# Kernel tuning notes

Hardware: AMD Instinct MI355X
Metric: run time of the kernel (lower is better)

Reference implementation:

```python
import jax, jax.numpy as jnp
import numpy as np

N_NODES = 100000


def _sage_conv(x, edge_index, W_l, W_r, b):
    # PyG SAGEConv (mean aggr): out_i = lin_l(mean_{j in N(i)} x_j) + lin_r(x_i)
    src, dst = edge_index[0], edge_index[1]
    msg = x[src]  # [E, d] gather
    agg_sum = jax.ops.segment_sum(msg, dst, num_segments=N_NODES)  # [N, d]
    deg = jax.ops.segment_sum(jnp.ones((src.shape[0],), x.dtype), dst, num_segments=N_NODES)
    agg = agg_sum / jnp.maximum(deg, 1.0)[:, None]  # mean aggregation
    return agg @ W_l.T + b + x @ W_r.T


def setup_inputs() -> dict:
    key = jax.random.key(0)
    k = jax.random.split(key, 8)
    d_in, hidden, out = 64, 128, 128
    x = jax.random.normal(k[0], (N_NODES, d_in), dtype=jnp.float32)
    edge_index = jax.random.randint(k[1], (2, 1600000), 0, N_NODES, dtype=jnp.int64)
    s1 = 1.0 / np.sqrt(d_in)
    s2 = 1.0 / np.sqrt(hidden)
    return {
        "x": x,
        "edge_index": edge_index,
        "W1_l": jax.random.uniform(k[2], (hidden, d_in), jnp.float32, -s1, s1),
        "W1_r": jax.random.uniform(k[3], (hidden, d_in), jnp.float32, -s1, s1),
        "b1": jnp.zeros((hidden,), jnp.float32),
        "W2_l": jax.random.uniform(k[4], (out, hidden), jnp.float32, -s2, s2),
        "W2_r": jax.random.uniform(k[5], (out, hidden), jnp.float32, -s2, s2),
        "b2": jnp.zeros((out,), jnp.float32),
    }


def reference(x, edge_index, W1_l, W1_r, b1, W2_l, W2_r, b2):
    h = jax.nn.relu(_sage_conv(x, edge_index, W1_l, W1_r, b1))
    return _sage_conv(h, edge_index, W2_l, W2_r, b2)
```

## Files before the change

kernel.cpp:

```cpp
#include <hip/hip_runtime.h>

#define NN 100000
#define NE 1600000
#define SCAN_BLK 2048

#define BSH 9
#define NBUCK2 ((NN + 511) / 512)
#define CHUNK 8192
#define NCHK ((NE + CHUNK - 1) / CHUNK)
#define L2T (NBUCK2 * NCHK)
#define NSTRIP (NN / 32)

using bf16x8 = __attribute__((ext_vector_type(8))) short;
using f32x16 = __attribute__((ext_vector_type(16))) float;

__device__ __forceinline__ unsigned short f2bf(float f) {
    unsigned u = __float_as_uint(f);
    u += 0x7FFFu + ((u >> 16) & 1u);
    return (unsigned short)(u >> 16);
}
__device__ __forceinline__ float bf2f(unsigned short h) {
    return __uint_as_float(((unsigned)h) << 16);
}

__global__ __launch_bounds__(256) void hist2_kernel(const int* __restrict__ dst,
                                                    int* __restrict__ histm) {
    __shared__ int lh[256];
    int blk = blockIdx.x, tid = threadIdx.x;
    lh[tid] = 0;
    __syncthreads();
    int base = blk * CHUNK;
#pragma unroll
    for (int t = 0; t < CHUNK / 256; t++) {
        int e = base + t * 256 + tid;
        if (e < NE) atomicAdd(&lh[dst[e] >> BSH], 1);
    }
    __syncthreads();
    if (tid < NBUCK2) histm[tid * NCHK + blk] = lh[tid];
}

__global__ __launch_bounds__(256) void scan1_kernel(int* __restrict__ data,
                                                    int* __restrict__ bsums, int L) {
    __shared__ int s[256];
    int bid = blockIdx.x, tid = threadIdx.x;
    int base = bid * SCAN_BLK + tid * 8;
    int v[8];
    int sum = 0;
#pragma unroll
    for (int t = 0; t < 8; t++) {
        int idx = base + t;
        v[t] = (idx < L) ? data[idx] : 0;
        sum += v[t];
    }
    s[tid] = sum;
    __syncthreads();
    for (int off = 1; off < 256; off <<= 1) {
        int val = (tid >= off) ? s[tid - off] : 0;
        __syncthreads();
        s[tid] += val;
        __syncthreads();
    }
    int excl = s[tid] - sum;
    if (tid == 255) bsums[bid] = s[255];
    int run = excl;
#pragma unroll
    for (int t = 0; t < 8; t++) {
        int idx = base + t;
        if (idx < L) data[idx] = run;
        run += v[t];
    }
}

__global__ __launch_bounds__(64) void scan2_kernel(int* __restrict__ bsums, int n) {
    int tid = threadIdx.x;
    int orig = (tid < n) ? bsums[tid] : 0;
    int v = orig;
    for (int off = 1; off < 64; off <<= 1) {
        int nb = __shfl_up(v, off, 64);
        if (tid >= off) v += nb;
    }
    if (tid < n) bsums[tid] = v - orig;
}

__global__ __launch_bounds__(256) void scan_add_kernel(int* __restrict__ data,
                                                       const int* __restrict__ bsums, int L) {
    int i = blockIdx.x * 256 + threadIdx.x;
    if (i < L) data[i] += bsums[i / SCAN_BLK];
}

__global__ __launch_bounds__(256) void scatter2_kernel(const int* __restrict__ src,
                                                       const int* __restrict__ dst,
                                                       const int* __restrict__ histm,
                                                       int* __restrict__ tmp) {
    __shared__ int lcur[256];
    int blk = blockIdx.x, tid = threadIdx.x;
    if (tid < NBUCK2) lcur[tid] = histm[tid * NCHK + blk];
    __syncthreads();
    int base = blk * CHUNK;
#pragma unroll
    for (int t = 0; t < CHUNK / 256; t++) {
        int e = base + t * 256 + tid;
        if (e < NE) {
            int d = dst[e];
            int p = atomicAdd(&lcur[d >> BSH], 1);
            tmp[p] = src[e] | ((d & 511) << 17);
        }
    }
}

__global__ __launch_bounds__(256) void count_place_kernel(const int* __restrict__ histm,
                                                          const int* __restrict__ tmp,
                                                          int* __restrict__ rowptr,
                                                          int* __restrict__ esrc) {
    __shared__ int cnt[512];
    __shared__ int s[256];
    int b = blockIdx.x, tid = threadIdx.x;
    int beg = histm[b * NCHK];
    int end = (b == NBUCK2 - 1) ? NE : histm[(b + 1) * NCHK];

    cnt[tid] = 0; cnt[tid + 256] = 0;
    __syncthreads();
    for (int e = beg + tid; e < end; e += 256)
        atomicAdd(&cnt[tmp[e] >> 17], 1);
    __syncthreads();

    int c0 = cnt[2 * tid], c1 = cnt[2 * tid + 1];
    int sum = c0 + c1;
    s[tid] = sum;
    __syncthreads();
    for (int off = 1; off < 256; off <<= 1) {
        int val = (tid >= off) ? s[tid - off] : 0;
        __syncthreads();
        s[tid] += val;
        __syncthreads();
    }
    int o0 = beg + s[tid] - sum;
    int o1 = o0 + c0;
    cnt[2 * tid] = o0;
    cnt[2 * tid + 1] = o1;
    int node0 = (b << BSH) + 2 * tid;
    if (node0 < NN)     rowptr[node0]     = o0;
    if (node0 + 1 < NN) rowptr[node0 + 1] = o1;
    if (b == 0 && tid == 0) rowptr[NN] = NE;
    __syncthreads();

    for (int e = beg + tid; e < end; e += 256) {
        int v = tmp[e];
        int p = atomicAdd(&cnt[v >> 17], 1);
        esrc[p] = v & 0x1FFFF;
    }
}

__global__ __launch_bounds__(256) void cvt_kernel(const float* __restrict__ in,
                                                  unsigned short* __restrict__ out, int n4) {
    int i = blockIdx.x * 256 + threadIdx.x;
    if (i < n4) {
        float4 f = ((const float4*)in)[i];
        ((ushort4*)out)[i] = make_ushort4(f2bf(f.x), f2bf(f.y), f2bf(f.z), f2bf(f.w));
    }
}

__global__ __launch_bounds__(256) void agg64_kernel(const unsigned short* __restrict__ feat,
                                                    const int* __restrict__ rowptr,
                                                    const int* __restrict__ esrc,
                                                    unsigned short* __restrict__ agg) {
    int node = blockIdx.x * 4 + (threadIdx.x >> 6);
    int lane = threadIdx.x & 63;
    int es = lane >> 3;
    int fi = lane & 7;
    int beg = rowptr[node], end = rowptr[node + 1];

    float ax[8];
#pragma unroll
    for (int i = 0; i < 8; i++) ax[i] = 0.0f;

    int e = beg;
    for (; e + 15 < end; e += 16) {
        int sA = esrc[e + es];
        int sB = esrc[e + 8 + es];
        bf16x8 uA = *(const bf16x8*)(feat + (size_t)sA * 64 + fi * 8);
        bf16x8 uB = *(const bf16x8*)(feat + (size_t)sB * 64 + fi * 8);
#pragma unroll
        for (int i = 0; i < 8; i++)
            ax[i] += bf2f((unsigned short)uA[i]) + bf2f((unsigned short)uB[i]);
    }
    if (e + 7 < end) {
        int s = esrc[e + es];
        bf16x8 u = *(const bf16x8*)(feat + (size_t)s * 64 + fi * 8);
#pragma unroll
        for (int i = 0; i < 8; i++) ax[i] += bf2f((unsigned short)u[i]);
        e += 8;
    }
    if (es < end - e) {
        int s = esrc[e + es];
        bf16x8 u = *(const bf16x8*)(feat + (size_t)s * 64 + fi * 8);
#pragma unroll
        for (int i = 0; i < 8; i++) ax[i] += bf2f((unsigned short)u[i]);
    }

#pragma unroll
    for (int i = 0; i < 8; i++) {
        ax[i] += __shfl_xor(ax[i], 8);
        ax[i] += __shfl_xor(ax[i], 16);
        ax[i] += __shfl_xor(ax[i], 32);
    }
    if (es == 0) {
        float inv = 1.0f / fmaxf((float)(end - beg), 1.0f);
        bf16x8 o;
#pragma unroll
        for (int i = 0; i < 8; i++) o[i] = (short)f2bf(ax[i] * inv);
        *(bf16x8*)(agg + (size_t)node * 64 + fi * 8) = o;
    }
}

__global__ __launch_bounds__(256) void agg128_kernel(const unsigned short* __restrict__ feat,
                                                     const int* __restrict__ rowptr,
                                                     const int* __restrict__ esrc,
                                                     unsigned short* __restrict__ agg) {
    int node = blockIdx.x * 4 + (threadIdx.x >> 6);
    int lane = threadIdx.x & 63;
    int es = lane >> 4;
    int fi = lane & 15;
    int beg = rowptr[node], end = rowptr[node + 1];

    float ax[8];
#pragma unroll
    for (int i = 0; i < 8; i++) ax[i] = 0.0f;

    int e = beg;
    for (; e + 15 < end; e += 16) {
        int s0 = esrc[e + es];
        int s1 = esrc[e + 4 + es];
        int s2 = esrc[e + 8 + es];
        int s3 = esrc[e + 12 + es];
        bf16x8 u0 = *(const bf16x8*)(feat + (size_t)s0 * 128 + fi * 8);
        bf16x8 u1 = *(const bf16x8*)(feat + (size_t)s1 * 128 + fi * 8);
        bf16x8 u2 = *(const bf16x8*)(feat + (size_t)s2 * 128 + fi * 8);
        bf16x8 u3 = *(const bf16x8*)(feat + (size_t)s3 * 128 + fi * 8);
#pragma unroll
        for (int i = 0; i < 8; i++)
            ax[i] += (bf2f((unsigned short)u0[i]) + bf2f((unsigned short)u1[i])) +
                     (bf2f((unsigned short)u2[i]) + bf2f((unsigned short)u3[i]));
    }
    for (; e + 3 < end; e += 4) {
        int s = esrc[e + es];
        bf16x8 u = *(const bf16x8*)(feat + (size_t)s * 128 + fi * 8);
#pragma unroll
        for (int i = 0; i < 8; i++) ax[i] += bf2f((unsigned short)u[i]);
    }
    if (es < end - e) {
        int s = esrc[e + es];
        bf16x8 u = *(const bf16x8*)(feat + (size_t)s * 128 + fi * 8);
#pragma unroll
        for (int i = 0; i < 8; i++) ax[i] += bf2f((unsigned short)u[i]);
    }

#pragma unroll
    for (int i = 0; i < 8; i++) {
        ax[i] += __shfl_xor(ax[i], 16);
        ax[i] += __shfl_xor(ax[i], 32);
    }
    if (es == 0) {
        float inv = 1.0f / fmaxf((float)(end - beg), 1.0f);
        bf16x8 o;
#pragma unroll
        for (int i = 0; i < 8; i++) o[i] = (short)f2bf(ax[i] * inv);
        *(bf16x8*)(agg + (size_t)node * 128 + fi * 8) = o;
    }
}

template <int K, bool RELU, bool OUTBF>
__global__ __launch_bounds__(256) void gemm_mfma_kernel(
    const unsigned short* __restrict__ A1,
    const unsigned short* __restrict__ A2,
    const unsigned short* __restrict__ Wa,
    const unsigned short* __restrict__ Wb,
    const float* __restrict__ bias,
    void* __restrict__ outv) {
    int strip = blockIdx.x * 4 + (threadIdx.x >> 6);
    if (strip >= NSTRIP) return;
    const int lane = threadIdx.x & 63;
    const int m = lane & 31;
    const int half = lane >> 5;
    const int base = strip * 32;

    f32x16 acc[4];
#pragma unroll
    for (int nb = 0; nb < 4; ++nb)
#pragma unroll
        for (int r = 0; r < 16; ++r) acc[nb][r] = 0.0f;

    const unsigned short* ar1 = A1 + (size_t)(base + m) * K + half * 8;
    const unsigned short* ar2 = A2 + (size_t)(base + m) * K + half * 8;
#pragma unroll
    for (int kc = 0; kc < K; kc += 16) {
        bf16x8 a = *(const bf16x8*)(ar1 + kc);
#pragma unroll
        for (int nb = 0; nb < 4; ++nb) {
            bf16x8 b = *(const bf16x8*)(Wa + (size_t)(nb * 32 + m) * K + kc + half * 8);
            acc[nb] = __builtin_amdgcn_mfma_f32_32x32x16_bf16(a, b, acc[nb], 0, 0, 0);
        }
    }
#pragma unroll
    for (int kc = 0; kc < K; kc += 16) {
        bf16x8 a = *(const bf16x8*)(ar2 + kc);
#pragma unroll
        for (int nb = 0; nb < 4; ++nb) {
            bf16x8 b = *(const bf16x8*)(Wb + (size_t)(nb * 32 + m) * K + kc + half * 8);
            acc[nb] = __builtin_amdgcn_mfma_f32_32x32x16_bf16(a, b, acc[nb], 0, 0, 0);
        }
    }

#pragma unroll
    for (int nb = 0; nb < 4; ++nb) {
        int j = nb * 32 + m;
        float bz = bias[j];
#pragma unroll
        for (int r = 0; r < 16; ++r) {
            int row = (r & 3) + 8 * (r >> 2) + 4 * half;
            float v = acc[nb][r] + bz;
            if (RELU) v = fmaxf(v, 0.0f);
            size_t idx = (size_t)(base + row) * 128 + j;
            if (OUTBF) ((unsigned short*)outv)[idx] = f2bf(v);
            else       ((float*)outv)[idx] = v;
        }
    }
}

extern "C" void kernel_launch(void* const* d_in, const int* in_sizes, int n_in,
                              void* d_out, int out_size, void* d_ws, size_t ws_size,
                              hipStream_t stream) {
    const float* x   = (const float*)d_in[0];
    const int*   ei  = (const int*)d_in[1];
    const float* W1l = (const float*)d_in[2];
    const float* W1r = (const float*)d_in[3];
    const float* b1  = (const float*)d_in[4];
    const float* W2l = (const float*)d_in[5];
    const float* W2r = (const float*)d_in[6];
    const float* b2  = (const float*)d_in[7];
    float* out = (float*)d_out;

    const int* src = ei;
    const int* dst = ei + NE;

    char* ws = (char*)d_ws;
    int* rowptr = (int*)ws;
    int* esrc   = (int*)(ws + 401408);
    unsigned short* aggB = (unsigned short*)(ws + 6803456);
    unsigned short* xb   = aggB + (size_t)NN * 64;
    char* E = ws + 32403456;
    unsigned short* hb = (unsigned short*)E;
    int* tmp   = (int*)E;
    int* histm = (int*)(E + 6400000);
    int* bsums = (int*)(E + 6560000);
    unsigned short* W1lb = (unsigned short*)d_out;
    unsigned short* W1rb = W1lb + 128 * 64;
    unsigned short* W2lb = (unsigned short*)ws;
    unsigned short* W2rb = W2lb + 128 * 128;

    const int GB  = (NSTRIP + 3) / 4;
    const int NSB2 = (L2T + SCAN_BLK - 1) / SCAN_BLK;

    hist2_kernel<<<NCHK, 256, 0, stream>>>(dst, histm);
    scan1_kernel<<<NSB2, 256, 0, stream>>>(histm, bsums, L2T);
    scan2_kernel<<<1, 64, 0, stream>>>(bsums, NSB2);
    scan_add_kernel<<<(L2T + 255) / 256, 256, 0, stream>>>(histm, bsums, L2T);
    scatter2_kernel<<<NCHK, 256, 0, stream>>>(src, dst, histm, tmp);
    count_place_kernel<<<NBUCK2, 256, 0, stream>>>(histm, tmp, rowptr, esrc);

    cvt_kernel<<<(NN * 64 / 4 + 255) / 256, 256, 0, stream>>>(x, xb, NN * 64 / 4);
    cvt_kernel<<<(128 * 64 / 4 + 255) / 256, 256, 0, stream>>>(W1l, W1lb, 128 * 64 / 4);
    cvt_kernel<<<(128 * 64 / 4 + 255) / 256, 256, 0, stream>>>(W1r, W1rb, 128 * 64 / 4);

    agg64_kernel<<<NN / 4, 256, 0, stream>>>(xb, rowptr, esrc, aggB);
    gemm_mfma_kernel<64, true, true><<<GB, 256, 0, stream>>>(aggB, xb, W1lb, W1rb, b1, hb);

    agg128_kernel<<<NN / 4, 256, 0, stream>>>(hb, rowptr, esrc, aggB);
    cvt_kernel<<<(128 * 128 / 4 + 255) / 256, 256, 0, stream>>>(W2l, W2lb, 128 * 128 / 4);
    cvt_kernel<<<(128 * 128 / 4 + 255) / 256, 256, 0, stream>>>(W2r, W2rb, 128 * 128 / 4);
    gemm_mfma_kernel<128, false, false><<<GB, 256, 0, stream>>>(aggB, hb, W2lb, W2rb, b2, out);
}
```

Baseline: 326.6 us.

## Single-block histogram scan, LDS-staged scatter, and fused weight conversion

The three-kernel prefix scan over the bucket histogram is replaced by one 1024-thread single-block scan. The scatter kernel now counts and locally sorts each chunk into LDS buckets before writing them out, so global writes are grouped by bucket instead of scattered per edge. The W1 conversions are merged into one cvtw kernel; it also writes W2 copies that go unused, because the W2 conversions are still launched separately before the second GEMM. This saves launches and improves write coalescing, at the cost of a serial per-thread scan loop and extra LDS use in the scatter kernel.

```diff
diff --git a/kernel.cpp b/kernel.cpp
--- a/kernel.cpp
+++ b/kernel.cpp
@@ -2,7 +2,6 @@
 
 #define NN 100000
 #define NE 1600000
-#define SCAN_BLK 2048
 
 #define BSH 9
 #define NBUCK2 ((NN + 511) / 512)
@@ -39,72 +38,78 @@
     if (tid < NBUCK2) histm[tid * NCHK + blk] = lh[tid];
 }
 
-__global__ __launch_bounds__(256) void scan1_kernel(int* __restrict__ data,
-                                                    int* __restrict__ bsums, int L) {
-    __shared__ int s[256];
-    int bid = blockIdx.x, tid = threadIdx.x;
-    int base = bid * SCAN_BLK + tid * 8;
-    int v[8];
+__global__ __launch_bounds__(1024) void scan_histm_kernel(int* __restrict__ data) {
+    __shared__ int s[1024];
+    const int PER = (L2T + 1023) / 1024;
+    int tid = threadIdx.x;
+    int lo = tid * PER;
+    int hi = lo + PER; if (hi > L2T) hi = L2T;
     int sum = 0;
-#pragma unroll
-    for (int t = 0; t < 8; t++) {
-        int idx = base + t;
-        v[t] = (idx < L) ? data[idx] : 0;
-        sum += v[t];
-    }
+    for (int i = lo; i < hi; i++) sum += data[i];
     s[tid] = sum;
     __syncthreads();
-    for (int off = 1; off < 256; off <<= 1) {
+    for (int off = 1; off < 1024; off <<= 1) {
         int val = (tid >= off) ? s[tid - off] : 0;
         __syncthreads();
         s[tid] += val;
         __syncthreads();
     }
-    int excl = s[tid] - sum;
-    if (tid == 255) bsums[bid] = s[255];
-    int run = excl;
-#pragma unroll
-    for (int t = 0; t < 8; t++) {
-        int idx = base + t;
-        if (idx < L) data[idx] = run;
-        run += v[t];
-    }
-}
-
-__global__ __launch_bounds__(64) void scan2_kernel(int* __restrict__ bsums, int n) {
-    int tid = threadIdx.x;
-    int orig = (tid < n) ? bsums[tid] : 0;
-    int v = orig;
-    for (int off = 1; off < 64; off <<= 1) {
-        int nb = __shfl_up(v, off, 64);
-        if (tid >= off) v += nb;
-    }
-    if (tid < n) bsums[tid] = v - orig;
-}
-
-__global__ __launch_bounds__(256) void scan_add_kernel(int* __restrict__ data,
-                                                       const int* __restrict__ bsums, int L) {
-    int i = blockIdx.x * 256 + threadIdx.x;
-    if (i < L) data[i] += bsums[i / SCAN_BLK];
+    int run = s[tid] - sum;
+    for (int i = lo; i < hi; i++) {
+        int d = data[i];
+        data[i] = run;
+        run += d;
+    }
 }
 
 __global__ __launch_bounds__(256) void scatter2_kernel(const int* __restrict__ src,
                                                        const int* __restrict__ dst,
                                                        const int* __restrict__ histm,
                                                        int* __restrict__ tmp) {
-    __shared__ int lcur[256];
+    __shared__ int staged[CHUNK];
+    __shared__ unsigned char stb[CHUNK];
+    __shared__ int cnt[NBUCK2];
+    __shared__ int loc[NBUCK2];
+    __shared__ int cur[NBUCK2];
+    __shared__ int segb[NBUCK2];
+    __shared__ int s[256];
     int blk = blockIdx.x, tid = threadIdx.x;
-    if (tid < NBUCK2) lcur[tid] = histm[tid * NCHK + blk];
-    __syncthreads();
     int base = blk * CHUNK;
-#pragma unroll
-    for (int t = 0; t < CHUNK / 256; t++) {
-        int e = base + t * 256 + tid;
-        if (e < NE) {
-            int d = dst[e];
-            int p = atomicAdd(&lcur[d >> BSH], 1);
-            tmp[p] = src[e] | ((d & 511) << 17);
-        }
+    int n = NE - base; if (n > CHUNK) n = CHUNK;
+
+    for (int i = tid; i < NBUCK2; i += 256) cnt[i] = 0;
+    __syncthreads();
+    for (int j = tid; j < n; j += 256)
+        atomicAdd(&cnt[dst[base + j] >> BSH], 1);
+    __syncthreads();
+    int c = (tid < NBUCK2) ? cnt[tid] : 0;
+    s[tid] = c;
+    __syncthreads();
+    for (int off = 1; off < 256; off <<= 1) {
+        int val = (tid >= off) ? s[tid - off] : 0;
+        __syncthreads();
+        s[tid] += val;
+        __syncthreads();
+    }
+    if (tid < NBUCK2) {
+        int ex = s[tid] - c;
+        loc[tid] = ex;
+        cur[tid] = ex;
+        segb[tid] = histm[tid * NCHK + blk];
+    }
+    __syncthreads();
+    for (int j = tid; j < n; j += 256) {
+        int d = dst[base + j];
+        int b = d >> BSH;
+        int v = src[base + j] | ((d & 511) << 17);
+        int r = atomicAdd(&cur[b], 1);
+        staged[r] = v;
+        stb[r] = (unsigned char)b;
+    }
+    __syncthreads();
+    for (int j = tid; j < n; j += 256) {
+        int b = stb[j];
+        tmp[segb[b] + (j - loc[b])] = staged[j];
     }
 }
 
@@ -158,6 +163,25 @@
         float4 f = ((const float4*)in)[i];
         ((ushort4*)out)[i] = make_ushort4(f2bf(f.x), f2bf(f.y), f2bf(f.z), f2bf(f.w));
     }
+}
+
+__global__ __launch_bounds__(256) void cvtw_kernel(const float* __restrict__ W1l,
+                                                   const float* __restrict__ W1r,
+                                                   const float* __restrict__ W2l,
+                                                   const float* __restrict__ W2r,
+                                                   unsigned short* __restrict__ W1lb,
+                                                   unsigned short* __restrict__ W1rb,
+                                                   unsigned short* __restrict__ W2lb,
+                                                   unsigned short* __restrict__ W2rb) {
+    const int N1 = 128 * 64 / 4, N2 = 128 * 128 / 4;
+    int j = blockIdx.x * 256 + threadIdx.x;
+    const float* in; unsigned short* out;
+    if (j < N1)              { in = W1l; out = W1lb; }
+    else if ((j -= N1) < N1) { in = W1r; out = W1rb; }
+    else if ((j -= N1) < N2) { in = W2l; out = W2lb; }
+    else                     { j -= N2; if (j >= N2) return; in = W2r; out = W2rb; }
+    float4 f = ((const float4*)in)[j];
+    ((ushort4*)out)[j] = make_ushort4(f2bf(f.x), f2bf(f.y), f2bf(f.z), f2bf(f.w));
 }
 
 __global__ __launch_bounds__(256) void agg64_kernel(const unsigned short* __restrict__ feat,
@@ -352,31 +376,35 @@
     unsigned short* hb = (unsigned short*)E;
     int* tmp   = (int*)E;
     int* histm = (int*)(E + 6400000);
-    int* bsums = (int*)(E + 6560000);
     unsigned short* W1lb = (unsigned short*)d_out;
     unsigned short* W1rb = W1lb + 128 * 64;
-    unsigned short* W2lb = (unsigned short*)ws;
-    unsigned short* W2rb = W2lb + 128 * 128;
+    unsigned short* W2lb;
+    unsigned short* W2rb;
+    {
+        unsigned short* wbase = (unsigned short*)(E + 6400000 + L2T * 4 + 256);
+        W2lb = wbase;
+        W2rb = wbase + 128 * 128;
+    }
 
     const int GB  = (NSTRIP + 3) / 4;
-    const int NSB2 = (L2T + SCAN_BLK - 1) / SCAN_BLK;
 
     hist2_kernel<<<NCHK, 256, 0, stream>>>(dst, histm);
-    scan1_kernel<<<NSB2, 256, 0, stream>>>(histm, bsums, L2T);
-    scan2_kernel<<<1, 64, 0, stream>>>(bsums, NSB2);
-    scan_add_kernel<<<(L2T + 255) / 256, 256, 0, stream>>>(histm, bsums, L2T);
+    scan_histm_kernel<<<1, 1024, 0, stream>>>(histm);
     scatter2_kernel<<<NCHK, 256, 0, stream>>>(src, dst, histm, tmp);
     count_place_kernel<<<NBUCK2, 256, 0, stream>>>(histm, tmp, rowptr, esrc);
 
     cvt_kernel<<<(NN * 64 / 4 + 255) / 256, 256, 0, stream>>>(x, xb, NN * 64 / 4);
-    cvt_kernel<<<(128 * 64 / 4 + 255) / 256, 256, 0, stream>>>(W1l, W1lb, 128 * 64 / 4);
-    cvt_kernel<<<(128 * 64 / 4 + 255) / 256, 256, 0, stream>>>(W1r, W1rb, 128 * 64 / 4);
+    cvtw_kernel<<<48, 256, 0, stream>>>(W1l, W1r, W2l, W2r, W1lb, W1rb, W2lb, W2rb);
 
     agg64_kernel<<<NN / 4, 256, 0, stream>>>(xb, rowptr, esrc, aggB);
     gemm_mfma_kernel<64, true, true><<<GB, 256, 0, stream>>>(aggB, xb, W1lb, W1rb, b1, hb);
 
     agg128_kernel<<<NN / 4, 256, 0, stream>>>(hb, rowptr, esrc, aggB);
-    cvt_kernel<<<(128 * 128 / 4 + 255) / 256, 256, 0, stream>>>(W2l, W2lb, 128 * 128 / 4);
-    cvt_kernel<<<(128 * 128 / 4 + 255) / 256, 256, 0, stream>>>(W2r, W2rb, 128 * 128 / 4);
-    gemm_mfma_kernel<128, false, false><<<GB, 256, 0, stream>>>(aggB, hb, W2lb, W2rb, b2, out);
-}
+    {
+        unsigned short* W2lb2 = (unsigned short*)ws;
+        unsigned short* W2rb2 = W2lb2 + 128 * 128;
+        cvt_kernel<<<(128 * 128 / 4 + 255) / 256, 256, 0, stream>>>(W2l, W2lb2, 128 * 128 / 4);
+        cvt_kernel<<<(128 * 128 / 4 + 255) / 256, 256, 0, stream>>>(W2r, W2rb2, 128 * 128 / 4);
+        gemm_mfma_kernel<128, false, false><<<GB, 256, 0, stream>>>(aggB, hb, W2lb2, W2rb2, b2, out);
+    }
+}
```

Result: slower. 365.8 us (+12.0%).
